# Performance work log

Hardware: AMD Instinct MI355X
Metric: run time of the kernel (lower is better)

## Reference

```python
import jax, jax.numpy as jnp
import numpy as np

D, NH, K = 768, 12, 2
B, T = 4, 2048
DH = D // NH
SCALE = float(np.sqrt(DH))


def setup_inputs() -> dict:
    key = jax.random.key(0)
    ks = jax.random.split(key, 9)
    H = jax.random.normal(ks[0], (B, T, D), dtype=jnp.float32)
    p = jax.random.uniform(ks[1], (B, T, K), dtype=jnp.float32)
    p = p / jnp.sum(p, axis=-1, keepdims=True)  # language probabilities
    s = jax.random.uniform(ks[2], (B, T), dtype=jnp.float32)
    w_init = 0.02
    wq = w_init * jax.random.normal(ks[3], (D, D), dtype=jnp.float32)
    wk = w_init * jax.random.normal(ks[4], (D, D), dtype=jnp.float32)
    wv = w_init * jax.random.normal(ks[5], (D, D), dtype=jnp.float32)
    wo = w_init * jax.random.normal(ks[6], (D, D), dtype=jnp.float32)
    bo = jnp.zeros((D,), dtype=jnp.float32)
    # per-head KxK compat matrices, init identity + small noise (as in torch code)
    compat = (jnp.broadcast_to(jnp.eye(K, dtype=jnp.float32), (NH, K, K))
              + 0.01 * jax.random.normal(ks[7], (NH, K, K), dtype=jnp.float32))
    gamma = 0.1 * jax.random.normal(ks[8], (1,), dtype=jnp.float32)
    return {"H": H, "p": p, "s": s, "wq": wq, "wk": wk, "wv": wv,
            "wo": wo, "bo": bo, "compat": compat, "gamma": gamma}


def _split(x):
    # (B,T,D) -> (B,NH,T,DH)
    b, t, _ = x.shape
    return x.reshape(b, t, NH, DH).transpose(0, 2, 1, 3)


def reference(H, p, s, wq, wk, wv, wo, bo, compat, gamma):
    # torch nn.Linear: y = x @ W.T  (weights stored (out,in))
    Q = _split(jnp.einsum('btd,ed->bte', H, wq))
    Kt = _split(jnp.einsum('btd,ed->bte', H, wk))
    V = _split(jnp.einsum('btd,ed->bte', H, wv))
    scores = jnp.einsum('bhid,bhjd->bhij', Q, Kt) / SCALE            # (B,H,T,T)
    p_compat = jnp.einsum('bik,hkl->bhil', p, compat)                 # (B,H,T,K)
    scores = scores + jnp.einsum('bhil,bjl->bhij', p_compat, p)       # bilinear lang bias
    scores = scores + gamma[0] * s[:, None, None, :]                  # position bias
    attn = jax.nn.softmax(scores, axis=-1)                            # dropout p=0 (eval)
    ctx = jnp.einsum('bhij,bhjd->bhid', attn, V)
    merged = ctx.transpose(0, 2, 1, 3).reshape(H.shape[0], H.shape[1], D)
    return jnp.einsum('btd,ed->bte', merged, wo) + bo
```

## Files before the change

### kernel.cpp

```cpp
#include <hip/hip_runtime.h>
#include <stdint.h>

#define TT 2048
#define DD 768
#define NHEAD 12
#define DH 64
#define MM 8192
#define DP 80

typedef __attribute__((ext_vector_type(8))) short bf16x8;
typedef __attribute__((ext_vector_type(4))) float f32x4;
typedef __attribute__((ext_vector_type(16))) float f32x16;
typedef __attribute__((ext_vector_type(2))) unsigned int u32x2v;
typedef unsigned short u16;

#define GAS __attribute__((address_space(1)))
#define LAS __attribute__((address_space(3)))

static __device__ __forceinline__ void gload16(const void* g, void* l) {
  __builtin_amdgcn_global_load_lds((const GAS uint32_t*)g, (LAS uint32_t*)l, 16, 0, 0);
}

static __device__ __forceinline__ u16 f2b(float f) {
  union { float f; uint32_t u; } x; x.f = f;
  uint32_t r = x.u + 0x7fffu + ((x.u >> 16) & 1u);
  return (u16)(r >> 16);
}
static __device__ __forceinline__ float b2f(u16 v) {
  union { uint32_t u; float f; } x; x.u = ((uint32_t)v) << 16; return x.f;
}

#if __has_builtin(__builtin_amdgcn_exp2f)
#define EXP2(x) __builtin_amdgcn_exp2f(x)
#else
#define EXP2(x) exp2f(x)
#endif

static __device__ __forceinline__ void pswap(uint32_t& a, uint32_t& b) {
#if __has_builtin(__builtin_amdgcn_permlane32_swap)
  u32x2v r = __builtin_amdgcn_permlane32_swap(a, b, false, false);
  a = r[0]; b = r[1];
#else
  uint32_t ax = (uint32_t)__shfl_xor((int)a, 32, 64);
  uint32_t bx = (uint32_t)__shfl_xor((int)b, 32, 64);
  bool lo = (threadIdx.x & 32) == 0;
  uint32_t na = lo ? a : bx, nb = lo ? ax : b;
  a = na; b = nb;
#endif
}
static __device__ __forceinline__ uint32_t cvtpk(float lo, float hi_) {
  uint32_t r;
  asm("v_cvt_pk_bf16_f32 %0, %1, %2" : "=v"(r) : "v"(lo), "v"(hi_));
  return r;
}
static __device__ __forceinline__ f32x16 mfma32(bf16x8 a, bf16x8 b, f32x16 c) {
  return __builtin_amdgcn_mfma_f32_32x32x16_bf16(a, b, c, 0, 0, 0);
}

__global__ __launch_bounds__(256) void convert_kernel(
    const float* __restrict__ H, const float* __restrict__ wq,
    const float* __restrict__ wk, const float* __restrict__ wv,
    const float* __restrict__ wo,
    const float* __restrict__ p, const float* __restrict__ s,
    const float* __restrict__ compat, const float* __restrict__ gamma,
    u16* __restrict__ Hb, u16* __restrict__ Wqkv, u16* __restrict__ Wob,
    u16* __restrict__ Qp, u16* __restrict__ Kp) {
  const size_t NHEL = (size_t)MM * DD;
  const size_t NW = (size_t)DD * DD;
  if (blockIdx.x >= 8448) {
    int i = (blockIdx.x - 8448) * 256 + threadIdx.x;
    if (i >= MM) return;
    int b = i >> 11, t = i & (TT - 1);
    const float L2E = 1.44269504f;
    float p0 = p[(size_t)i * 2], p1 = p[(size_t)i * 2 + 1], sv = s[i];
    u16 p0h = f2b(p0); u16 p0l = f2b(p0 - b2f(p0h));
    u16 p1h = f2b(p1); u16 p1l = f2b(p1 - b2f(p1h));
    u16 svh = f2b(sv); u16 svl = f2b(sv - b2f(svh));
    u16 gmb = f2b(gamma[0] * L2E);
    union { u16 u[8]; uint4 v; } kv, qv, zz;
#pragma unroll
    for (int z = 0; z < 8; ++z) zz.u[z] = 0;
    kv.u[0] = p0h; kv.u[1] = p0l; kv.u[2] = p1h; kv.u[3] = p1l;
    kv.u[4] = svh; kv.u[5] = svl; kv.u[6] = 0; kv.u[7] = 0;
#pragma unroll
    for (int h = 0; h < NHEAD; ++h) {
      float c00 = compat[h * 4 + 0], c01 = compat[h * 4 + 1];
      float c10 = compat[h * 4 + 2], c11 = compat[h * 4 + 3];
      u16 q0 = f2b((p0 * c00 + p1 * c10) * L2E);
      u16 q1 = f2b((p0 * c01 + p1 * c11) * L2E);
      qv.u[0] = q0; qv.u[1] = q0; qv.u[2] = q1; qv.u[3] = q1;
      qv.u[4] = gmb; qv.u[5] = gmb; qv.u[6] = 0; qv.u[7] = 0;
      size_t row = ((size_t)(b * NHEAD + h) * TT + t) * DP;
      *(uint4*)&Qp[row + 64] = qv.v;
      *(uint4*)&Qp[row + 72] = zz.v;
      *(uint4*)&Kp[row + 64] = kv.v;
      *(uint4*)&Kp[row + 72] = zz.v;
    }
    return;
  }
  size_t i = ((size_t)blockIdx.x * 256 + threadIdx.x) * 4;
  const float* src; u16* dst; size_t so, dofs;
  if (i < NHEL) { src = H; so = i; dst = Hb; dofs = i; }
  else if (i < NHEL + 3 * NW) {
    size_t j = i - NHEL; dst = Wqkv; dofs = j;
    if (j < NW) { src = wq; so = j; }
    else if (j < 2 * NW) { src = wk; so = j - NW; }
    else { src = wv; so = j - 2 * NW; }
  } else if (i < NHEL + 4 * NW) {
    size_t j = i - NHEL - 3 * NW; src = wo; so = j; dst = Wob; dofs = j;
  } else return;
  float4 v = *(const float4*)&src[so];
  ushort4 o;
  o.x = f2b(v.x); o.y = f2b(v.y); o.z = f2b(v.z); o.w = f2b(v.w);
  *(ushort4*)&dst[dofs] = o;
}

template <int MODE>
__global__ __launch_bounds__(256) void gemm_kernel(
    const u16* __restrict__ A, const u16* __restrict__ Bw,
    u16* __restrict__ Qp, u16* __restrict__ Kp, u16* __restrict__ Vt,
    const float* __restrict__ bo, float* __restrict__ Out) {
  __shared__ u16 SMEM[17408];
  u16* As = SMEM;
  u16* Bs = SMEM + 8192;
  const int tid = threadIdx.x;
  const int lane = tid & 63, w = tid >> 6;
  const int wr = w >> 1, wc = w & 1;
  const int g = lane >> 4, r = lane & 15;
  const int m0 = blockIdx.x * 128, n0 = blockIdx.y * 128;

  f32x4 acc[4][4];
#pragma unroll
  for (int m = 0; m < 4; ++m)
#pragma unroll
    for (int n = 0; n < 4; ++n) acc[m][n] = (f32x4){0.f, 0.f, 0.f, 0.f};

  for (int ks = 0; ks < 12; ++ks) {
    const int k0 = ks * 64;
    __syncthreads();
#pragma unroll
    for (int ii = 0; ii < 4; ++ii) {
      int seg = (w * 4 + ii) * 64 + lane;
      int row = seg >> 3, cs = seg & 7;
      int csw = cs ^ (row & 7);
      gload16(&A[(size_t)(m0 + row) * DD + k0 + csw * 8], &As[(w * 4 + ii) * 512]);
      gload16(&Bw[(size_t)(n0 + row) * DD + k0 + csw * 8], &Bs[(w * 4 + ii) * 512]);
    }
    __syncthreads();
#pragma unroll
    for (int kk = 0; kk < 2; ++kk) {
      bf16x8 af[4], bfr[4];
#pragma unroll
      for (int m = 0; m < 4; ++m) {
        int row = wr * 64 + m * 16 + r;
        int ch = (kk * 4 + g) ^ (row & 7);
        af[m] = *(const bf16x8*)&As[row * 64 + ch * 8];
      }
#pragma unroll
      for (int n = 0; n < 4; ++n) {
        int row = wc * 64 + n * 16 + r;
        int ch = (kk * 4 + g) ^ (row & 7);
        bfr[n] = *(const bf16x8*)&Bs[row * 64 + ch * 8];
      }
#pragma unroll
      for (int m = 0; m < 4; ++m)
#pragma unroll
        for (int n = 0; n < 4; ++n)
          acc[m][n] = __builtin_amdgcn_mfma_f32_16x16x32_bf16(af[m], bfr[n], acc[m][n], 0, 0, 0);
    }
  }

  if (MODE == 0) {
    const int sel = n0 / DD;
    const int e0b = n0 - sel * DD;
    const int bb = m0 >> 11;
    const int tb = m0 & (TT - 1);
    __syncthreads();
#pragma unroll
    for (int m = 0; m < 4; ++m) {
#pragma unroll
      for (int n = 0; n < 4; ++n) {
#pragma unroll
        for (int reg = 0; reg < 4; ++reg) {
          float v = acc[m][n][reg];
          int t = wr * 64 + m * 16 + g * 4 + reg;
          int c = wc * 64 + n * 16 + r;
          u16 bv = f2b(sel == 0 ? v * 0.18033688f : v);
          if (sel < 2) SMEM[t * 136 + c] = bv;
          else         SMEM[c * 136 + t] = bv;
        }
      }
    }
    __syncthreads();
    if (sel < 2) {
      u16* base = (sel == 0) ? Qp : Kp;
      const int grp = tid >> 3, li = tid & 7;
#pragma unroll
      for (int it = 0; it < 8; ++it) {
        int chunk = it * 32 + grp;
        int t = chunk & 127, hh = chunk >> 7;
        int h = (e0b >> 6) + hh;
        size_t row = ((size_t)(bb * NHEAD + h) * TT + tb + t) * DP;
        uint4 d = *(const uint4*)&SMEM[t * 136 + hh * 64 + li * 8];
        *(uint4*)&base[row + li * 8] = d;
      }
    } else {
      const int grp = tid >> 4, li = tid & 15;
#pragma unroll
      for (int it = 0; it < 8; ++it) {
        int c = it * 16 + grp;
        int h = (e0b >> 6) + (c >> 6), dh = c & 63;
        size_t row = ((size_t)(bb * NHEAD + h)) * DH * TT + (size_t)dh * TT + tb;
        uint4 d = *(const uint4*)&SMEM[c * 136 + li * 8];
        *(uint4*)&Vt[row + li * 8] = d;
      }
    }
  } else {
#pragma unroll
    for (int m = 0; m < 4; ++m) {
#pragma unroll
      for (int n = 0; n < 4; ++n) {
#pragma unroll
        for (int reg = 0; reg < 4; ++reg) {
          int gt = m0 + wr * 64 + m * 16 + g * 4 + reg;
          int e = n0 + wc * 64 + n * 16 + r;
          Out[(size_t)gt * DD + e] = acc[m][n][reg] + bo[e];
        }
      }
    }
  }
}

#define QBLK 128
__global__ __launch_bounds__(128, 2) void attn_kernel(
    const u16* __restrict__ Qp, const u16* __restrict__ Kp, const u16* __restrict__ Vtb,
    u16* __restrict__ Ctx) {
  __shared__ u16 Ks[2][64 * 88];
  __shared__ u16 Vs[2][64 * 64];
  const int tid = threadIdx.x, lane = tid & 63, w = tid >> 6;
  const int hi = lane >> 5, ql = lane & 31;
  const int bid = blockIdx.x;
  const int bh = bid % 48, qb = bid / 48;
  const int b = bh / NHEAD, h = bh % NHEAD;

  const char* KgB = (const char*)(Kp + (size_t)bh * TT * DP);
  const char* VgB = (const char*)(Vtb + (size_t)bh * DH * TT);
  const u16* Qg = Qp + (size_t)bh * TT * DP;

  const int q0r = qb * QBLK + w * 64 + ql;
  bf16x8 Qf0[5], Qf1[5];
#pragma unroll
  for (int kbl = 0; kbl < 5; ++kbl) {
    Qf0[kbl] = *(const bf16x8*)&Qg[(size_t)q0r * DP + (2 * kbl + hi) * 8];
    Qf1[kbl] = *(const bf16x8*)&Qg[(size_t)(q0r + 32) * DP + (2 * kbl + hi) * 8];
  }

  union { u16 u[8]; bf16x8 v; } ones;
#pragma unroll
  for (int z = 0; z < 8; ++z) ones.u[z] = 0x3F80;

  auto STAGE = [&](int nb, int t0) {
    const char* ksrc = KgB + (size_t)t0 * 160;
    char* kd = (char*)&Ks[nb][0];
#pragma unroll
    for (int i = 0; i < 5; ++i) {
      int n = (i * 2 + w) * 64 + lane;
      int rr = (n * 2979) >> 15;
      int c = n - 11 * rr; if (c > 9) c = 9;
      gload16(ksrc + rr * 160 + c * 16, kd + (i * 2 + w) * 1024);
    }
    if (w == 0) {
      int n = 640 + lane;
      int rr = (n * 2979) >> 15;
      int c = n - 11 * rr; if (c > 9) c = 9;
      gload16(ksrc + rr * 160 + c * 16, kd + 10240);
    }
    const char* vsrc = VgB + (size_t)t0 * 2;
    char* vd = (char*)&Vs[nb][0];
#pragma unroll
    for (int j = 0; j < 4; ++j) {
      int n = (j * 2 + w) * 64 + lane;
      int dh = n >> 3, cs = n & 7;
      gload16(vsrc + dh * 4096 + ((cs ^ (dh & 7))) * 16, vd + (j * 2 + w) * 1024);
    }
  };

  f32x16 o00, o01, o10, o11, ol0, ol1;
#pragma unroll
  for (int z = 0; z < 16; ++z) {
    o00[z] = 0.f; o01[z] = 0.f; o10[z] = 0.f; o11[z] = 0.f; ol0[z] = 0.f; ol1[z] = 0.f;
  }

  STAGE(0, 0);

  for (int kt = 0; kt < 32; ++kt) {
    __syncthreads();
    if (kt + 1 < 32) STAGE((kt + 1) & 1, (kt + 1) * 64);
    const u16* Kb_ = &Ks[kt & 1][0];
    const u16* Vb_ = &Vs[kt & 1][0];

    f32x16 s00, s01, s10, s11;
#pragma unroll
    for (int z = 0; z < 16; ++z) { s00[z] = 0.f; s01[z] = 0.f; s10[z] = 0.f; s11[z] = 0.f; }
    __builtin_amdgcn_s_setprio(1);
#pragma unroll
    for (int kbl = 0; kbl < 5; ++kbl) {
      bf16x8 kf0 = *(const bf16x8*)&Kb_[ql * 88 + hi * 8 + kbl * 16];
      bf16x8 kf1 = *(const bf16x8*)&Kb_[(ql + 32) * 88 + hi * 8 + kbl * 16];
      s00 = mfma32(kf0, Qf0[kbl], s00);
      s01 = mfma32(kf0, Qf1[kbl], s01);
      s10 = mfma32(kf1, Qf0[kbl], s10);
      s11 = mfma32(kf1, Qf1[kbl], s11);
    }
    __builtin_amdgcn_s_setprio(0);

    bf16x8 pa0[4], pa1[4];
#pragma unroll
    for (int half = 0; half < 2; ++half) {
      float p_[32];
      if (half == 0) {
#pragma unroll
        for (int z = 0; z < 16; ++z) { p_[z] = EXP2(s00[z]); p_[16 + z] = EXP2(s10[z]); }
      } else {
#pragma unroll
        for (int z = 0; z < 16; ++z) { p_[z] = EXP2(s01[z]); p_[16 + z] = EXP2(s11[z]); }
      }
#pragma unroll
      for (int ks = 0; ks < 4; ++ks) {
        const int base = ks * 8;
        uint32_t wa = cvtpk(p_[base + 0], p_[base + 1]);
        uint32_t wb = cvtpk(p_[base + 4], p_[base + 5]);
        uint32_t wc = cvtpk(p_[base + 2], p_[base + 3]);
        uint32_t wd = cvtpk(p_[base + 6], p_[base + 7]);
        pswap(wa, wb);
        pswap(wc, wd);
        union { uint32_t u[4]; bf16x8 v; } pa;
        pa.u[0] = wa; pa.u[1] = wc; pa.u[2] = wb; pa.u[3] = wd;
        if (half == 0) pa0[ks] = pa.v; else pa1[ks] = pa.v;
      }
    }

    __builtin_amdgcn_s_setprio(1);
#pragma unroll
    for (int ks = 0; ks < 4; ++ks) {
      const int sw = ((2 * ks + hi) ^ (ql & 7)) * 8;
      bf16x8 vf0 = *(const bf16x8*)&Vb_[ql * 64 + sw];
      bf16x8 vf1 = *(const bf16x8*)&Vb_[(ql + 32) * 64 + sw];
      o00 = mfma32(pa0[ks], vf0, o00);
      o10 = mfma32(pa1[ks], vf0, o10);
      o01 = mfma32(pa0[ks], vf1, o01);
      o11 = mfma32(pa1[ks], vf1, o11);
      ol0 = mfma32(pa0[ks], ones.v, ol0);
      ol1 = mfma32(pa1[ks], ones.v, ol1);
    }
    __builtin_amdgcn_s_setprio(0);
  }

#pragma unroll
  for (int z = 0; z < 16; ++z) {
    int q2 = (z & 3) + 8 * (z >> 2) + 4 * hi;
    int qrow0 = qb * QBLK + w * 64 + q2;
    float il0 = 1.0f / ol0[z];
    size_t rowb0 = ((size_t)b * TT + qrow0) * DD + h * DH;
    Ctx[rowb0 + ql]      = f2b(o00[z] * il0);
    Ctx[rowb0 + ql + 32] = f2b(o01[z] * il0);
    float il1 = 1.0f / ol1[z];
    size_t rowb1 = rowb0 + 32 * DD;
    Ctx[rowb1 + ql]      = f2b(o10[z] * il1);
    Ctx[rowb1 + ql + 32] = f2b(o11[z] * il1);
  }
}

extern "C" void kernel_launch(void* const* d_in, const int* in_sizes, int n_in,
                              void* d_out, int out_size, void* d_ws, size_t ws_size,
                              hipStream_t stream) {
  const float* H = (const float*)d_in[0];
  const float* p = (const float*)d_in[1];
  const float* s = (const float*)d_in[2];
  const float* wq = (const float*)d_in[3];
  const float* wk = (const float*)d_in[4];
  const float* wv = (const float*)d_in[5];
  const float* wo = (const float*)d_in[6];
  const float* bo = (const float*)d_in[7];
  const float* compat = (const float*)d_in[8];
  const float* gamma = (const float*)d_in[9];
  float* out = (float*)d_out;

  char* ws = (char*)d_ws;
  u16* Hb   = (u16*)(ws);
  u16* Wqkv = (u16*)(ws + 12582912);
  u16* Wob  = (u16*)(ws + 16121856);
  u16* Qpb  = (u16*)(ws + 17301504);
  u16* Kpb  = (u16*)(ws + 33030144);
  u16* Vtb  = (u16*)(ws + 48758784);
  u16* Ctx  = Hb;

  convert_kernel<<<8480, 256, 0, stream>>>(H, wq, wk, wv, wo, p, s, compat, gamma,
                                           Hb, Wqkv, Wob, Qpb, Kpb);
  gemm_kernel<0><<<dim3(64, 18), 256, 0, stream>>>(Hb, Wqkv, Qpb, Kpb, Vtb, nullptr, nullptr);
  attn_kernel<<<768, 128, 0, stream>>>(Qpb, Kpb, Vtb, Ctx);
  gemm_kernel<1><<<dim3(64, 6), 256, 0, stream>>>(Ctx, Wob, nullptr, nullptr, nullptr, bo, out);
}
```

Before: 169.0 us.

## Split attention key tiles across two wave pairs and reduce partial outputs via LDS

The attention kernel moves from 2 to 4 waves per block. Each pair of waves takes half of every 64-key tile for the same 64 queries, and the kh=1 waves hand their partial output accumulators and row sums to the kh=0 waves through shared memory at the end. Row sums are now built from scalar adds of the exponentials instead of extra MFMAs against a ones vector. The aim is more wavefronts in flight to hide latency, and fewer MFMA instructions per tile. The cost is an extra cross-wave reduction through LDS with two more barriers, and K/V staging is spread over four waves.

```diff
diff --git a/kernel.cpp b/kernel.cpp
--- a/kernel.cpp
+++ b/kernel.cpp
@@ -232,12 +232,17 @@
 }
 
 #define QBLK 128
-__global__ __launch_bounds__(128, 2) void attn_kernel(
+__global__ __launch_bounds__(256, 3) void attn_kernel(
     const u16* __restrict__ Qp, const u16* __restrict__ Kp, const u16* __restrict__ Vtb,
     u16* __restrict__ Ctx) {
-  __shared__ u16 Ks[2][64 * 88];
-  __shared__ u16 Vs[2][64 * 64];
+  __shared__ char SMC[38912];
+  u16* KsBase = (u16*)SMC;
+  u16* VsBase = (u16*)(SMC + 22528);
+  float* OsF = (float*)SMC;
+  float* LsF = (float*)(SMC + 32768);
+
   const int tid = threadIdx.x, lane = tid & 63, w = tid >> 6;
+  const int qg = w & 1, kh = w >> 1;
   const int hi = lane >> 5, ql = lane & 31;
   const int bid = blockIdx.x;
   const int bh = bid % 48, qb = bid / 48;
@@ -247,7 +252,7 @@
   const char* VgB = (const char*)(Vtb + (size_t)bh * DH * TT);
   const u16* Qg = Qp + (size_t)bh * TT * DP;
 
-  const int q0r = qb * QBLK + w * 64 + ql;
+  const int q0r = qb * QBLK + qg * 64 + ql;
   bf16x8 Qf0[5], Qf1[5];
 #pragma unroll
   for (int kbl = 0; kbl < 5; ++kbl) {
@@ -255,119 +260,140 @@
     Qf1[kbl] = *(const bf16x8*)&Qg[(size_t)(q0r + 32) * DP + (2 * kbl + hi) * 8];
   }
 
-  union { u16 u[8]; bf16x8 v; } ones;
-#pragma unroll
-  for (int z = 0; z < 8; ++z) ones.u[z] = 0x3F80;
-
   auto STAGE = [&](int nb, int t0) {
     const char* ksrc = KgB + (size_t)t0 * 160;
-    char* kd = (char*)&Ks[nb][0];
-#pragma unroll
-    for (int i = 0; i < 5; ++i) {
-      int n = (i * 2 + w) * 64 + lane;
-      int rr = (n * 2979) >> 15;
-      int c = n - 11 * rr; if (c > 9) c = 9;
-      gload16(ksrc + rr * 160 + c * 16, kd + (i * 2 + w) * 1024);
-    }
-    if (w == 0) {
-      int n = 640 + lane;
-      int rr = (n * 2979) >> 15;
-      int c = n - 11 * rr; if (c > 9) c = 9;
-      gload16(ksrc + rr * 160 + c * 16, kd + 10240);
+    char* kd = (char*)(KsBase + nb * (64 * 88));
+#pragma unroll
+    for (int i = 0; i < 3; ++i) {
+      int idx = w + 4 * i;
+      if (idx < 11) {
+        int n = idx * 64 + lane;
+        int rr = (n * 2979) >> 15;
+        int c = n - 11 * rr; if (c > 9) c = 9;
+        gload16(ksrc + rr * 160 + c * 16, kd + idx * 1024);
+      }
     }
     const char* vsrc = VgB + (size_t)t0 * 2;
-    char* vd = (char*)&Vs[nb][0];
-#pragma unroll
-    for (int j = 0; j < 4; ++j) {
-      int n = (j * 2 + w) * 64 + lane;
+    char* vd = (char*)(VsBase + nb * (64 * 64));
+#pragma unroll
+    for (int j = 0; j < 2; ++j) {
+      int idx = w + 4 * j;
+      int n = idx * 64 + lane;
       int dh = n >> 3, cs = n & 7;
-      gload16(vsrc + dh * 4096 + ((cs ^ (dh & 7))) * 16, vd + (j * 2 + w) * 1024);
+      gload16(vsrc + dh * 4096 + ((cs ^ (dh & 7))) * 16, vd + idx * 1024);
     }
   };
 
-  f32x16 o00, o01, o10, o11, ol0, ol1;
-#pragma unroll
-  for (int z = 0; z < 16; ++z) {
-    o00[z] = 0.f; o01[z] = 0.f; o10[z] = 0.f; o11[z] = 0.f; ol0[z] = 0.f; ol1[z] = 0.f;
-  }
+  f32x16 o00, o01, o10, o11;
+#pragma unroll
+  for (int z = 0; z < 16; ++z) { o00[z] = 0.f; o01[z] = 0.f; o10[z] = 0.f; o11[z] = 0.f; }
+  float l0 = 0.f, l1 = 0.f;
 
   STAGE(0, 0);
 
   for (int kt = 0; kt < 32; ++kt) {
     __syncthreads();
     if (kt + 1 < 32) STAGE((kt + 1) & 1, (kt + 1) * 64);
-    const u16* Kb_ = &Ks[kt & 1][0];
-    const u16* Vb_ = &Vs[kt & 1][0];
-
-    f32x16 s00, s01, s10, s11;
-#pragma unroll
-    for (int z = 0; z < 16; ++z) { s00[z] = 0.f; s01[z] = 0.f; s10[z] = 0.f; s11[z] = 0.f; }
+    const u16* Kb_ = KsBase + (kt & 1) * (64 * 88);
+    const u16* Vb_ = VsBase + (kt & 1) * (64 * 64);
+
+    f32x16 s0, s1;
+#pragma unroll
+    for (int z = 0; z < 16; ++z) { s0[z] = 0.f; s1[z] = 0.f; }
     __builtin_amdgcn_s_setprio(1);
 #pragma unroll
     for (int kbl = 0; kbl < 5; ++kbl) {
-      bf16x8 kf0 = *(const bf16x8*)&Kb_[ql * 88 + hi * 8 + kbl * 16];
-      bf16x8 kf1 = *(const bf16x8*)&Kb_[(ql + 32) * 88 + hi * 8 + kbl * 16];
-      s00 = mfma32(kf0, Qf0[kbl], s00);
-      s01 = mfma32(kf0, Qf1[kbl], s01);
-      s10 = mfma32(kf1, Qf0[kbl], s10);
-      s11 = mfma32(kf1, Qf1[kbl], s11);
+      bf16x8 kf = *(const bf16x8*)&Kb_[(kh * 32 + ql) * 88 + hi * 8 + kbl * 16];
+      s0 = mfma32(kf, Qf0[kbl], s0);
+      s1 = mfma32(kf, Qf1[kbl], s1);
     }
     __builtin_amdgcn_s_setprio(0);
 
-    bf16x8 pa0[4], pa1[4];
-#pragma unroll
-    for (int half = 0; half < 2; ++half) {
-      float p_[32];
-      if (half == 0) {
-#pragma unroll
-        for (int z = 0; z < 16; ++z) { p_[z] = EXP2(s00[z]); p_[16 + z] = EXP2(s10[z]); }
-      } else {
-#pragma unroll
-        for (int z = 0; z < 16; ++z) { p_[z] = EXP2(s01[z]); p_[16 + z] = EXP2(s11[z]); }
-      }
-#pragma unroll
-      for (int ks = 0; ks < 4; ++ks) {
-        const int base = ks * 8;
-        uint32_t wa = cvtpk(p_[base + 0], p_[base + 1]);
-        uint32_t wb = cvtpk(p_[base + 4], p_[base + 5]);
-        uint32_t wc = cvtpk(p_[base + 2], p_[base + 3]);
-        uint32_t wd = cvtpk(p_[base + 6], p_[base + 7]);
-        pswap(wa, wb);
-        pswap(wc, wd);
+    float p0_[16], p1_[16];
+#pragma unroll
+    for (int z = 0; z < 16; ++z) { p0_[z] = EXP2(s0[z]); p1_[z] = EXP2(s1[z]); }
+    float t0s = 0.f, t1s = 0.f;
+#pragma unroll
+    for (int z = 0; z < 16; ++z) { t0s += p0_[z]; t1s += p1_[z]; }
+    l0 += t0s; l1 += t1s;
+
+    bf16x8 pa0[2], pa1[2];
+#pragma unroll
+    for (int ks = 0; ks < 2; ++ks) {
+      const int base = ks * 8;
+      {
+        uint32_t wa = cvtpk(p0_[base + 0], p0_[base + 1]);
+        uint32_t wb = cvtpk(p0_[base + 4], p0_[base + 5]);
+        uint32_t wc = cvtpk(p0_[base + 2], p0_[base + 3]);
+        uint32_t wd = cvtpk(p0_[base + 6], p0_[base + 7]);
+        pswap(wa, wb); pswap(wc, wd);
         union { uint32_t u[4]; bf16x8 v; } pa;
         pa.u[0] = wa; pa.u[1] = wc; pa.u[2] = wb; pa.u[3] = wd;
-        if (half == 0) pa0[ks] = pa.v; else pa1[ks] = pa.v;
+        pa0[ks] = pa.v;
+      }
+      {
+        uint32_t wa = cvtpk(p1_[base + 0], p1_[base + 1]);
+        uint32_t wb = cvtpk(p1_[base + 4], p1_[base + 5]);
+        uint32_t wc = cvtpk(p1_[base + 2], p1_[base + 3]);
+        uint32_t wd = cvtpk(p1_[base + 6], p1_[base + 7]);
+        pswap(wa, wb); pswap(wc, wd);
+        union { uint32_t u[4]; bf16x8 v; } pa;
+        pa.u[0] = wa; pa.u[1] = wc; pa.u[2] = wb; pa.u[3] = wd;
+        pa1[ks] = pa.v;
       }
     }
 
     __builtin_amdgcn_s_setprio(1);
 #pragma unroll
-    for (int ks = 0; ks < 4; ++ks) {
-      const int sw = ((2 * ks + hi) ^ (ql & 7)) * 8;
+    for (int ks = 0; ks < 2; ++ks) {
+      const int sw = ((2 * (kh * 2 + ks) + hi) ^ (ql & 7)) * 8;
       bf16x8 vf0 = *(const bf16x8*)&Vb_[ql * 64 + sw];
       bf16x8 vf1 = *(const bf16x8*)&Vb_[(ql + 32) * 64 + sw];
       o00 = mfma32(pa0[ks], vf0, o00);
       o10 = mfma32(pa1[ks], vf0, o10);
       o01 = mfma32(pa0[ks], vf1, o01);
       o11 = mfma32(pa1[ks], vf1, o11);
-      ol0 = mfma32(pa0[ks], ones.v, ol0);
-      ol1 = mfma32(pa1[ks], ones.v, ol1);
     }
     __builtin_amdgcn_s_setprio(0);
   }
 
-#pragma unroll
-  for (int z = 0; z < 16; ++z) {
-    int q2 = (z & 3) + 8 * (z >> 2) + 4 * hi;
-    int qrow0 = qb * QBLK + w * 64 + q2;
-    float il0 = 1.0f / ol0[z];
-    size_t rowb0 = ((size_t)b * TT + qrow0) * DD + h * DH;
-    Ctx[rowb0 + ql]      = f2b(o00[z] * il0);
-    Ctx[rowb0 + ql + 32] = f2b(o01[z] * il0);
-    float il1 = 1.0f / ol1[z];
-    size_t rowb1 = rowb0 + 32 * DD;
-    Ctx[rowb1 + ql]      = f2b(o10[z] * il1);
-    Ctx[rowb1 + ql + 32] = f2b(o11[z] * il1);
+  __syncthreads();
+  if (kh == 1) {
+#pragma unroll
+    for (int z = 0; z < 16; ++z) {
+      int q2 = (z & 3) + 8 * (z >> 2) + 4 * hi;
+      OsF[(qg * 64 + q2) * 64 + ql]           = o00[z];
+      OsF[(qg * 64 + q2) * 64 + ql + 32]      = o01[z];
+      OsF[(qg * 64 + 32 + q2) * 64 + ql]      = o10[z];
+      OsF[(qg * 64 + 32 + q2) * 64 + ql + 32] = o11[z];
+    }
+  }
+  LsF[(qg * 64 + ql) * 4 + kh * 2 + hi]      = l0;
+  LsF[(qg * 64 + 32 + ql) * 4 + kh * 2 + hi] = l1;
+  __syncthreads();
+  if (kh == 0) {
+#pragma unroll
+    for (int z = 0; z < 16; ++z) {
+      int q2 = (z & 3) + 8 * (z >> 2) + 4 * hi;
+      float lt0 = LsF[(qg * 64 + q2) * 4 + 0] + LsF[(qg * 64 + q2) * 4 + 1]
+                + LsF[(qg * 64 + q2) * 4 + 2] + LsF[(qg * 64 + q2) * 4 + 3];
+      float il0 = 1.0f / lt0;
+      float a00 = o00[z] + OsF[(qg * 64 + q2) * 64 + ql];
+      float a01 = o01[z] + OsF[(qg * 64 + q2) * 64 + ql + 32];
+      int qrow0 = qb * QBLK + qg * 64 + q2;
+      size_t rowb0 = ((size_t)b * TT + qrow0) * DD + h * DH;
+      Ctx[rowb0 + ql]      = f2b(a00 * il0);
+      Ctx[rowb0 + ql + 32] = f2b(a01 * il0);
+      int lq1 = 32 + q2;
+      float lt1 = LsF[(qg * 64 + lq1) * 4 + 0] + LsF[(qg * 64 + lq1) * 4 + 1]
+                + LsF[(qg * 64 + lq1) * 4 + 2] + LsF[(qg * 64 + lq1) * 4 + 3];
+      float il1 = 1.0f / lt1;
+      float a10 = o10[z] + OsF[(qg * 64 + lq1) * 64 + ql];
+      float a11 = o11[z] + OsF[(qg * 64 + lq1) * 64 + ql + 32];
+      size_t rowb1 = rowb0 + 32 * DD;
+      Ctx[rowb1 + ql]      = f2b(a10 * il1);
+      Ctx[rowb1 + ql + 32] = f2b(a11 * il1);
+    }
   }
 }
 
@@ -398,6 +424,6 @@
   convert_kernel<<<8480, 256, 0, stream>>>(H, wq, wk, wv, wo, p, s, compat, gamma,
                                            Hb, Wqkv, Wob, Qpb, Kpb);
   gemm_kernel<0><<<dim3(64, 18), 256, 0, stream>>>(Hb, Wqkv, Qpb, Kpb, Vtb, nullptr, nullptr);
-  attn_kernel<<<768, 128, 0, stream>>>(Qpb, Kpb, Vtb, Ctx);
+  attn_kernel<<<768, 256, 0, stream>>>(Qpb, Kpb, Vtb, Ctx);
   gemm_kernel<1><<<dim3(64, 6), 256, 0, stream>>>(Ctx, Wob, nullptr, nullptr, nullptr, bo, out);
 }
```

After: 161.7 us. 1.04x faster.
